# Kernel optimization log

Hardware: AMD Instinct MI355X
Metric: run time of the kernel (lower is better)

Reference implementation:

```python
import jax, jax.numpy as jnp
import numpy as np

B, H, P, S = 512, 4, 196, 256  # batch, heads, pixels, states
D = S // H  # head_state = 64


def conv1x1(x, w, b):
    # x: (B, C_in, P), w: (C_out, C_in), b: (C_out,) -> (B, C_out, P)
    return jnp.einsum('oc,bcp->bop', w, x) + b[None, :, None]


def setup_inputs() -> dict:
    key = jax.random.key(0)
    ks = jax.random.split(key, 9)
    sc = 1.0 / np.sqrt(S)
    return {
        'x': jax.random.normal(ks[0], (B, S, P), dtype=jnp.float32),
        'wq': jax.random.normal(ks[1], (S, S), dtype=jnp.float32) * sc,
        'bq': jax.random.normal(ks[2], (S,), dtype=jnp.float32) * 0.01,
        'wk': jax.random.normal(ks[3], (S, S), dtype=jnp.float32) * sc,
        'bk': jax.random.normal(ks[4], (S,), dtype=jnp.float32) * 0.01,
        'wv': jax.random.normal(ks[5], (S, S), dtype=jnp.float32) * sc,
        'bv': jax.random.normal(ks[6], (S,), dtype=jnp.float32) * 0.01,
        'wo': jax.random.normal(ks[7], (S, S), dtype=jnp.float32) * sc,
        'bo': jax.random.normal(ks[8], (S,), dtype=jnp.float32) * 0.01,
    }


def reference(x, wq, bq, wk, bk, wv, bv, wo, bo):
    def split_heads(t):  # (B, S, P) -> (B, H, P, D)
        return t.reshape(B, H, D, P).swapaxes(-1, -2)

    q = split_heads(conv1x1(x, wq, bq))
    k = split_heads(conv1x1(x, wk, bk))
    v = split_heads(conv1x1(x, wv, bv))

    att = jnp.einsum('bhqd,bhkd->bhqk', q, k) / np.sqrt(D).astype(jnp.float32)
    att = jax.nn.softmax(att, axis=-1)
    av = jnp.einsum('bhqk,bhkd->bhqd', att, v)  # (B, H, P, D)

    # Faithful to original: raw view (B,H,P,D) -> (B,P,S) with NO head transpose
    merged = av.reshape(B, P, S).swapaxes(-1, -2)  # (B, S, P)
    return conv1x1(merged, wo, bo)
```

## Files before the change

kernel.cpp:

```cpp
#include <hip/hip_runtime.h>
#include <stdint.h>


#define PPIX 196
#define SS   256
#define PPAD 224
#define NTT  14

typedef __attribute__((ext_vector_type(8))) short short8;
typedef __attribute__((ext_vector_type(4))) float f32x4;

#define SZ_REGA 29696
#define OFF_QS  (SZ_REGA)
#define SZ_QKS  (224*72*2)
#define OFF_KS  (OFF_QS + SZ_QKS)
#define OFF_VS  (OFF_KS + SZ_QKS)
#define SZ_VS   (64*232*2)
#define OFF_AVS (OFF_VS + SZ_VS)
#define SZ_AVS  32768
#define SMEM_TOTAL (OFF_AVS + SZ_AVS)

static __device__ __forceinline__ uint16_t f2b(float f) {
  uint32_t u = __float_as_uint(f);
  return (uint16_t)((u + 0x7fffu + ((u >> 16) & 1u)) >> 16);
}
static __device__ __forceinline__ f32x4 fz4() {
  f32x4 v; v[0] = 0.f; v[1] = 0.f; v[2] = 0.f; v[3] = 0.f; return v;
}

extern "C" __global__ void __launch_bounds__(256, 1)
mha_fused(const float* __restrict__ x,
          const float* __restrict__ wq, const float* __restrict__ bq,
          const float* __restrict__ wk, const float* __restrict__ bk,
          const float* __restrict__ wv, const float* __restrict__ bv,
          const float* __restrict__ wo, const float* __restrict__ bo,
          float* __restrict__ out) {
  extern __shared__ char smem[];
  uint16_t* const regA = (uint16_t*)(smem);
  uint16_t* const qs   = (uint16_t*)(smem + OFF_QS);
  uint16_t* const ks   = (uint16_t*)(smem + OFF_KS);
  uint16_t* const vsm  = (uint16_t*)(smem + OFF_VS);
  uint16_t* const avs  = (uint16_t*)(smem + OFF_AVS);

  const int bid = blockIdx.x;
  const int L = (bid & 7) * 256 + (bid >> 3);
  const int b = L >> 2, h = L & 3;
  const int tid = threadIdx.x;
  const int w = tid >> 6;
  const int lane = tid & 63;
  const int g = lane >> 4;
  const int l15 = lane & 15;

  const float* xb = x + (size_t)b * (SS * PPIX);

  f32x4 acc1[3][NTT];
#pragma unroll
  for (int mi = 0; mi < 3; ++mi)
#pragma unroll
    for (int nt = 0; nt < NTT; ++nt) acc1[mi][nt] = fz4();

  for (int cc = 0; cc < 4; ++cc) {
    __syncthreads();
    if (tid < PPAD) {
      const int p = tid;
      const int swz = (p & 7) << 3;
      uint32_t* dst = (uint32_t*)(regA + p * 64);
      if (p < PPIX) {
        const float* src = xb + (size_t)(cc * 64) * PPIX + p;
#pragma unroll
        for (int i = 0; i < 32; ++i) {
          float a0 = src[(2 * i) * PPIX];
          float a1 = src[(2 * i + 1) * PPIX];
          uint32_t pk = (uint32_t)f2b(a0) | ((uint32_t)f2b(a1) << 16);
          dst[((2 * i) ^ swz) >> 1] = pk;
        }
      } else {
#pragma unroll
        for (int i = 0; i < 32; ++i) dst[((2 * i) ^ swz) >> 1] = 0u;
      }
    }
    __syncthreads();
#pragma unroll
    for (int kt = 0; kt < 2; ++kt) {
      short8 afr[3];
#pragma unroll
      for (int mi = 0; mi < 3; ++mi) {
        const int mt = 3 * w + mi;
        const int chA = 16 * mt + l15;
        const int mat = chA >> 6;
        const int dA = chA & 63;
        const float* W = (mat == 0) ? wq : ((mat == 1) ? wk : wv);
        const float* srcA = W + (size_t)(h * 64 + dA) * SS + cc * 64 + kt * 32 + g * 8;
        f32x4 w0 = *(const f32x4*)srcA;
        f32x4 w1 = *(const f32x4*)(srcA + 4);
        short8 af;
#pragma unroll
        for (int j = 0; j < 4; ++j) { af[j] = (short)f2b(w0[j]); af[4 + j] = (short)f2b(w1[j]); }
        afr[mi] = af;
      }
#pragma unroll
      for (int nt = 0; nt < NTT; ++nt) {
        const int p = 16 * nt + l15;
        const int coff = (kt * 32 + g * 8) ^ ((p & 7) << 3);
        short8 bfr = *(const short8*)(regA + p * 64 + coff);
#pragma unroll
        for (int mi = 0; mi < 3; ++mi)
          acc1[mi][nt] = __builtin_amdgcn_mfma_f32_16x16x32_bf16(afr[mi], bfr, acc1[mi][nt], 0, 0, 0);
      }
    }
  }
#pragma unroll
  for (int mi = 0; mi < 3; ++mi) {
    const int mt = 3 * w + mi;
    const int mat = (16 * mt) >> 6;
    const float* bias = (mat == 0) ? bq : ((mat == 1) ? bk : bv);
#pragma unroll
    for (int r = 0; r < 4; ++r) {
      const int ch = 16 * mt + 4 * g + r;
      const int d = ch - 64 * mat;
      const float bias_v = bias[h * 64 + d];
#pragma unroll
      for (int nt = 0; nt < NTT; ++nt) {
        const int p = 16 * nt + l15;
        const uint16_t val = f2b(acc1[mi][nt][r] + bias_v);
        if (mat == 2)      vsm[d * 232 + p] = val;
        else if (mat == 0) qs[p * 72 + d]   = val;
        else               ks[p * 72 + d]   = val;
      }
    }
  }
  __syncthreads();

  uint16_t* const psw = regA + w * (16 * 232);
  for (int rt = w; rt < NTT; rt += 4) {
    if (16 * rt >= PPIX) continue;
    f32x4 accA[NTT];
#pragma unroll
    for (int nt = 0; nt < NTT; ++nt) accA[nt] = fz4();
#pragma unroll
    for (int kt = 0; kt < 2; ++kt) {
      short8 a = *(const short8*)(qs + (16 * rt + l15) * 72 + kt * 32 + g * 8);
#pragma unroll
      for (int nt = 0; nt < NTT; ++nt) {
        short8 bfr = *(const short8*)(ks + (16 * nt + l15) * 72 + kt * 32 + g * 8);
        accA[nt] = __builtin_amdgcn_mfma_f32_16x16x32_bf16(a, bfr, accA[nt], 0, 0, 0);
      }
    }
    float mx[4] = {-1e30f, -1e30f, -1e30f, -1e30f};
#pragma unroll
    for (int nt = 0; nt < NTT; ++nt) {
      const int col = 16 * nt + l15;
#pragma unroll
      for (int r = 0; r < 4; ++r) {
        float v = accA[nt][r] * 0.125f;
        if (col >= PPIX) v = -1e30f;
        accA[nt][r] = v;
        mx[r] = fmaxf(mx[r], v);
      }
    }
#pragma unroll
    for (int off = 1; off <= 8; off <<= 1)
#pragma unroll
      for (int r = 0; r < 4; ++r)
        mx[r] = fmaxf(mx[r], __shfl_xor(mx[r], off, 64));
    float sm[4] = {0.f, 0.f, 0.f, 0.f};
#pragma unroll
    for (int nt = 0; nt < NTT; ++nt)
#pragma unroll
      for (int r = 0; r < 4; ++r) {
        float e = exp2f((accA[nt][r] - mx[r]) * 1.44269504088896f);
        accA[nt][r] = e;
        sm[r] += e;
      }
#pragma unroll
    for (int off = 1; off <= 8; off <<= 1)
#pragma unroll
      for (int r = 0; r < 4; ++r)
        sm[r] += __shfl_xor(sm[r], off, 64);
#pragma unroll
    for (int nt = 0; nt < NTT; ++nt)
#pragma unroll
      for (int r = 0; r < 4; ++r)
        psw[(4 * g + r) * 232 + 16 * nt + l15] = f2b(accA[nt][r]);
    f32x4 accV[4];
#pragma unroll
    for (int n = 0; n < 4; ++n) accV[n] = fz4();
#pragma unroll
    for (int kt = 0; kt < 7; ++kt) {
      short8 a = *(const short8*)(psw + l15 * 232 + kt * 32 + g * 8);
#pragma unroll
      for (int n = 0; n < 4; ++n) {
        short8 bfr = *(const short8*)(vsm + (16 * n + l15) * 232 + kt * 32 + g * 8);
        accV[n] = __builtin_amdgcn_mfma_f32_16x16x32_bf16(a, bfr, accV[n], 0, 0, 0);
      }
    }
#pragma unroll
    for (int r = 0; r < 4; ++r) {
      const int p = 16 * rt + 4 * g + r;
      if (p < PPIX) {
        const float inv = 1.0f / sm[r];
        const int swzp = ((p >> 2) & 7) << 3;
#pragma unroll
        for (int n = 0; n < 4; ++n) {
          const int d = 16 * n + l15;
          avs[p * 64 + (d ^ swzp)] = f2b(accV[n][r] * inv);
        }
      }
    }
  }
  __syncthreads();

  f32x4 accO[4][4];
#pragma unroll
  for (int mi = 0; mi < 4; ++mi)
#pragma unroll
    for (int ni = 0; ni < 4; ++ni) accO[mi][ni] = fz4();
#pragma unroll
  for (int kt = 0; kt < 8; ++kt) {
    short8 a[4];
#pragma unroll
    for (int mi = 0; mi < 4; ++mi) {
      const int o = 64 * w + 16 * mi + l15;
      const float* srcA = wo + (size_t)o * SS + kt * 32 + g * 8;
      f32x4 w0 = *(const f32x4*)srcA;
      f32x4 w1 = *(const f32x4*)(srcA + 4);
      short8 af;
#pragma unroll
      for (int j = 0; j < 4; ++j) { af[j] = (short)f2b(w0[j]); af[4 + j] = (short)f2b(w1[j]); }
      a[mi] = af;
    }
#pragma unroll
    for (int ni = 0; ni < 4; ++ni) {
      const int pp = 16 * ni + l15;
      const int s0 = kt * 32 + g * 8;
      const int idx = 256 * pp + ((s0 >> 6) << 6) + ((s0 & 63) ^ ((pp & 7) << 3));
      short8 bfr = *(const short8*)(avs + idx);
#pragma unroll
      for (int mi = 0; mi < 4; ++mi)
        accO[mi][ni] = __builtin_amdgcn_mfma_f32_16x16x32_bf16(a[mi], bfr, accO[mi][ni], 0, 0, 0);
    }
  }
#pragma unroll
  for (int mi = 0; mi < 4; ++mi) {
#pragma unroll
    for (int r = 0; r < 4; ++r) {
      const int o = 64 * w + 16 * mi + 4 * g + r;
      const float bias_v = bo[o];
      float* orow = out + ((size_t)b * SS + o) * PPIX + 49 * h;
#pragma unroll
      for (int ni = 0; ni < 4; ++ni) {
        const int pp = 16 * ni + l15;
        if (pp < 49) orow[pp] = accO[mi][ni][r] + bias_v;
      }
    }
  }
}

extern "C" void kernel_launch(void* const* d_in, const int* in_sizes, int n_in,
                              void* d_out, int out_size, void* d_ws, size_t ws_size,
                              hipStream_t stream) {
  (void)in_sizes; (void)n_in; (void)d_ws; (void)ws_size; (void)out_size;
  const float* x  = (const float*)d_in[0];
  const float* wq = (const float*)d_in[1];
  const float* bq = (const float*)d_in[2];
  const float* wk = (const float*)d_in[3];
  const float* bk = (const float*)d_in[4];
  const float* wv = (const float*)d_in[5];
  const float* bv = (const float*)d_in[6];
  const float* wo = (const float*)d_in[7];
  const float* bo = (const float*)d_in[8];
  float* out = (float*)d_out;
  (void)hipFuncSetAttribute(reinterpret_cast<const void*>(mha_fused),
                            hipFuncAttributeMaxDynamicSharedMemorySize, SMEM_TOTAL);
  mha_fused<<<dim3(2048), dim3(256), SMEM_TOTAL, stream>>>(x, wq, bq, wk, bk, wv, bv, wo, bo, out);
}
```

Baseline: 616.3 us.

## Double threads per block, prepack bf16 weights, and shrink LDS for two blocks per CU

Blocks go from 256 to 512 threads, and the QKV projection work is split across pixel halves as well as channel tiles. The out-projection is split across 8 warps. LDS is shrunk (smaller padded Q/K/V buffers, half-split P staging with a swizzle) so two blocks fit per CU, with launch bounds raised to (512,2). A prepack kernel converts all weights to bf16 in workspace once per call, so the main kernel loads bf16 directly instead of converting fp32 per block. The softmax scale is folded into the exp2 constant. The trade-off is more register pressure per thread and one extra kernel launch.

```diff
diff --git a/kernel.cpp b/kernel.cpp
--- a/kernel.cpp
+++ b/kernel.cpp
@@ -4,20 +4,19 @@
 
 #define PPIX 196
 #define SS   256
-#define PPAD 224
-#define NTT  14
 
 typedef __attribute__((ext_vector_type(8))) short short8;
 typedef __attribute__((ext_vector_type(4))) float f32x4;
 
-#define SZ_REGA 29696
-#define OFF_QS  (SZ_REGA)
-#define SZ_QKS  (224*72*2)
-#define OFF_KS  (OFF_QS + SZ_QKS)
-#define OFF_VS  (OFF_KS + SZ_QKS)
-#define SZ_VS   (64*232*2)
+#define PSWP    144
+#define SZ_UNI  36864
+#define OFF_QS  (SZ_UNI)
+#define SZ_QK   (208*72*2)
+#define OFF_KS  (OFF_QS + SZ_QK)
+#define OFF_VS  (OFF_KS + SZ_QK)
+#define SZ_VS   (64*236*2)
 #define OFF_AVS (OFF_VS + SZ_VS)
-#define SZ_AVS  32768
+#define SZ_AVS  (12544*2)
 #define SMEM_TOTAL (OFF_AVS + SZ_AVS)
 
 static __device__ __forceinline__ uint16_t f2b(float f) {
@@ -28,19 +27,21 @@
   f32x4 v; v[0] = 0.f; v[1] = 0.f; v[2] = 0.f; v[3] = 0.f; return v;
 }
 
-extern "C" __global__ void __launch_bounds__(256, 1)
-mha_fused(const float* __restrict__ x,
-          const float* __restrict__ wq, const float* __restrict__ bq,
-          const float* __restrict__ wk, const float* __restrict__ bk,
-          const float* __restrict__ wv, const float* __restrict__ bv,
-          const float* __restrict__ wo, const float* __restrict__ bo,
-          float* __restrict__ out) {
+template<bool PRE>
+__global__ __launch_bounds__(512, 2)
+void mha_fused(const float* __restrict__ x,
+               const float* __restrict__ wq, const float* __restrict__ bq,
+               const float* __restrict__ wk, const float* __restrict__ bk,
+               const float* __restrict__ wv, const float* __restrict__ bv,
+               const float* __restrict__ wo, const float* __restrict__ bo,
+               const uint16_t* __restrict__ wpk,
+               float* __restrict__ out) {
   extern __shared__ char smem[];
-  uint16_t* const regA = (uint16_t*)(smem);
-  uint16_t* const qs   = (uint16_t*)(smem + OFF_QS);
-  uint16_t* const ks   = (uint16_t*)(smem + OFF_KS);
-  uint16_t* const vsm  = (uint16_t*)(smem + OFF_VS);
-  uint16_t* const avs  = (uint16_t*)(smem + OFF_AVS);
+  uint16_t* const uni = (uint16_t*)(smem);
+  uint16_t* const qs  = (uint16_t*)(smem + OFF_QS);
+  uint16_t* const ks  = (uint16_t*)(smem + OFF_KS);
+  uint16_t* const vsm = (uint16_t*)(smem + OFF_VS);
+  uint16_t* const avs = (uint16_t*)(smem + OFF_AVS);
 
   const int bid = blockIdx.x;
   const int L = (bid & 7) * 256 + (bid >> 3);
@@ -50,110 +51,123 @@
   const int lane = tid & 63;
   const int g = lane >> 4;
   const int l15 = lane & 15;
+  const int wm = w & 3;
+  const int wn = w >> 2;
 
   const float* xb = x + (size_t)b * (SS * PPIX);
 
-  f32x4 acc1[3][NTT];
+  f32x4 acc1[3][7];
 #pragma unroll
   for (int mi = 0; mi < 3; ++mi)
 #pragma unroll
-    for (int nt = 0; nt < NTT; ++nt) acc1[mi][nt] = fz4();
+    for (int nt = 0; nt < 7; ++nt) acc1[mi][nt] = fz4();
+
+  const int prow = tid >> 1;
+  const int phalf = tid & 1;
 
   for (int cc = 0; cc < 4; ++cc) {
     __syncthreads();
-    if (tid < PPAD) {
-      const int p = tid;
-      const int swz = (p & 7) << 3;
-      uint32_t* dst = (uint32_t*)(regA + p * 64);
-      if (p < PPIX) {
-        const float* src = xb + (size_t)(cc * 64) * PPIX + p;
-#pragma unroll
-        for (int i = 0; i < 32; ++i) {
-          float a0 = src[(2 * i) * PPIX];
-          float a1 = src[(2 * i + 1) * PPIX];
-          uint32_t pk = (uint32_t)f2b(a0) | ((uint32_t)f2b(a1) << 16);
-          dst[((2 * i) ^ swz) >> 1] = pk;
+    short8 afr[2][3];
+#pragma unroll
+    for (int kt = 0; kt < 2; ++kt)
+#pragma unroll
+      for (int mi = 0; mi < 3; ++mi) {
+        const int chA = 48 * wm + 16 * mi + l15;
+        const int mat = chA >> 6, dA = chA & 63;
+        const int col = cc * 64 + kt * 32 + g * 8;
+        if (PRE) {
+          afr[kt][mi] = *(const short8*)(wpk + ((size_t)(mat * 256 + h * 64 + dA)) * SS + col);
+        } else {
+          const float* W = (mat == 0) ? wq : ((mat == 1) ? wk : wv);
+          const float* s = W + (size_t)(h * 64 + dA) * SS + col;
+          f32x4 w0 = *(const f32x4*)s, w1 = *(const f32x4*)(s + 4);
+          short8 af;
+#pragma unroll
+          for (int j = 0; j < 4; ++j) { af[j] = (short)f2b(w0[j]); af[4 + j] = (short)f2b(w1[j]); }
+          afr[kt][mi] = af;
+        }
+      }
+    if (prow < 224) {
+      const int swz = (prow & 7) << 3;
+      uint16_t* dstrow = uni + prow * 64;
+      if (prow < PPIX) {
+        const float* src = xb + (size_t)(cc * 64 + phalf * 32) * PPIX + prow;
+#pragma unroll
+        for (int cb = 0; cb < 4; ++cb) {
+          short8 pk;
+#pragma unroll
+          for (int t = 0; t < 8; ++t) pk[t] = (short)f2b(src[(cb * 8 + t) * PPIX]);
+          *(short8*)(dstrow + ((phalf * 32 + cb * 8) ^ swz)) = pk;
         }
       } else {
-#pragma unroll
-        for (int i = 0; i < 32; ++i) dst[((2 * i) ^ swz) >> 1] = 0u;
+        short8 z;
+#pragma unroll
+        for (int t = 0; t < 8; ++t) z[t] = 0;
+#pragma unroll
+        for (int cb = 0; cb < 4; ++cb)
+          *(short8*)(dstrow + ((phalf * 32 + cb * 8) ^ swz)) = z;
       }
     }
     __syncthreads();
 #pragma unroll
-    for (int kt = 0; kt < 2; ++kt) {
-      short8 afr[3];
-#pragma unroll
-      for (int mi = 0; mi < 3; ++mi) {
-        const int mt = 3 * w + mi;
-        const int chA = 16 * mt + l15;
-        const int mat = chA >> 6;
-        const int dA = chA & 63;
-        const float* W = (mat == 0) ? wq : ((mat == 1) ? wk : wv);
-        const float* srcA = W + (size_t)(h * 64 + dA) * SS + cc * 64 + kt * 32 + g * 8;
-        f32x4 w0 = *(const f32x4*)srcA;
-        f32x4 w1 = *(const f32x4*)(srcA + 4);
-        short8 af;
-#pragma unroll
-        for (int j = 0; j < 4; ++j) { af[j] = (short)f2b(w0[j]); af[4 + j] = (short)f2b(w1[j]); }
-        afr[mi] = af;
-      }
-#pragma unroll
-      for (int nt = 0; nt < NTT; ++nt) {
-        const int p = 16 * nt + l15;
+    for (int kt = 0; kt < 2; ++kt)
+#pragma unroll
+      for (int ntl = 0; ntl < 7; ++ntl) {
+        const int p = 16 * (7 * wn + ntl) + l15;
         const int coff = (kt * 32 + g * 8) ^ ((p & 7) << 3);
-        short8 bfr = *(const short8*)(regA + p * 64 + coff);
+        short8 bfr = *(const short8*)(uni + p * 64 + coff);
 #pragma unroll
         for (int mi = 0; mi < 3; ++mi)
-          acc1[mi][nt] = __builtin_amdgcn_mfma_f32_16x16x32_bf16(afr[mi], bfr, acc1[mi][nt], 0, 0, 0);
-      }
-    }
+          acc1[mi][ntl] = __builtin_amdgcn_mfma_f32_16x16x32_bf16(afr[kt][mi], bfr, acc1[mi][ntl], 0, 0, 0);
+      }
   }
 #pragma unroll
   for (int mi = 0; mi < 3; ++mi) {
-    const int mt = 3 * w + mi;
-    const int mat = (16 * mt) >> 6;
+    const int ch0 = 48 * wm + 16 * mi;
+    const int mat = ch0 >> 6;
     const float* bias = (mat == 0) ? bq : ((mat == 1) ? bk : bv);
 #pragma unroll
     for (int r = 0; r < 4; ++r) {
-      const int ch = 16 * mt + 4 * g + r;
-      const int d = ch - 64 * mat;
+      const int ch = ch0 + 4 * g + r;
+      const int d = ch & 63;
       const float bias_v = bias[h * 64 + d];
 #pragma unroll
-      for (int nt = 0; nt < NTT; ++nt) {
-        const int p = 16 * nt + l15;
-        const uint16_t val = f2b(acc1[mi][nt][r] + bias_v);
-        if (mat == 2)      vsm[d * 232 + p] = val;
-        else if (mat == 0) qs[p * 72 + d]   = val;
-        else               ks[p * 72 + d]   = val;
+      for (int ntl = 0; ntl < 7; ++ntl) {
+        const int p = 16 * (7 * wn + ntl) + l15;
+        const uint16_t val = f2b(acc1[mi][ntl][r] + bias_v);
+        if (mat == 2)      vsm[d * 236 + p] = val;
+        else if (mat == 0) { if (p < 208) qs[p * 72 + d] = val; }
+        else               { if (p < 208) ks[p * 72 + d] = val; }
       }
     }
   }
   __syncthreads();
 
-  uint16_t* const psw = regA + w * (16 * 232);
-  for (int rt = w; rt < NTT; rt += 4) {
-    if (16 * rt >= PPIX) continue;
-    f32x4 accA[NTT];
-#pragma unroll
-    for (int nt = 0; nt < NTT; ++nt) accA[nt] = fz4();
+  uint16_t* const psw = uni + w * (16 * PSWP);
+#pragma unroll 1
+  for (int round = 0; round < 2; ++round) {
+    const int rt = 8 * round + w;
+    if (rt > 12) continue;
+    f32x4 accA[14];
+#pragma unroll
+    for (int nt = 0; nt < 14; ++nt) accA[nt] = fz4();
 #pragma unroll
     for (int kt = 0; kt < 2; ++kt) {
       short8 a = *(const short8*)(qs + (16 * rt + l15) * 72 + kt * 32 + g * 8);
 #pragma unroll
-      for (int nt = 0; nt < NTT; ++nt) {
+      for (int nt = 0; nt < 14; ++nt) {
         short8 bfr = *(const short8*)(ks + (16 * nt + l15) * 72 + kt * 32 + g * 8);
         accA[nt] = __builtin_amdgcn_mfma_f32_16x16x32_bf16(a, bfr, accA[nt], 0, 0, 0);
       }
     }
-    float mx[4] = {-1e30f, -1e30f, -1e30f, -1e30f};
-#pragma unroll
-    for (int nt = 0; nt < NTT; ++nt) {
+    float mx[4] = {-3e38f, -3e38f, -3e38f, -3e38f};
+#pragma unroll
+    for (int nt = 0; nt < 14; ++nt) {
       const int col = 16 * nt + l15;
 #pragma unroll
       for (int r = 0; r < 4; ++r) {
-        float v = accA[nt][r] * 0.125f;
-        if (col >= PPIX) v = -1e30f;
+        float v = accA[nt][r];
+        if (col >= PPIX) v = -3e38f;
         accA[nt][r] = v;
         mx[r] = fmaxf(mx[r], v);
       }
@@ -164,11 +178,12 @@
       for (int r = 0; r < 4; ++r)
         mx[r] = fmaxf(mx[r], __shfl_xor(mx[r], off, 64));
     float sm[4] = {0.f, 0.f, 0.f, 0.f};
-#pragma unroll
-    for (int nt = 0; nt < NTT; ++nt)
+    const float cs = 0.125f * 1.44269504088896f;
+#pragma unroll
+    for (int nt = 0; nt < 14; ++nt)
 #pragma unroll
       for (int r = 0; r < 4; ++r) {
-        float e = exp2f((accA[nt][r] - mx[r]) * 1.44269504088896f);
+        float e = exp2f((accA[nt][r] - mx[r]) * cs);
         accA[nt][r] = e;
         sm[r] += e;
       }
@@ -177,20 +192,39 @@
 #pragma unroll
       for (int r = 0; r < 4; ++r)
         sm[r] += __shfl_xor(sm[r], off, 64);
-#pragma unroll
-    for (int nt = 0; nt < NTT; ++nt)
-#pragma unroll
-      for (int r = 0; r < 4; ++r)
-        psw[(4 * g + r) * 232 + 16 * nt + l15] = f2b(accA[nt][r]);
+
     f32x4 accV[4];
 #pragma unroll
     for (int n = 0; n < 4; ++n) accV[n] = fz4();
 #pragma unroll
-    for (int kt = 0; kt < 7; ++kt) {
-      short8 a = *(const short8*)(psw + l15 * 232 + kt * 32 + g * 8);
+    for (int nt = 0; nt < 8; ++nt)
+#pragma unroll
+      for (int r = 0; r < 4; ++r) {
+        const int row = 4 * g + r;
+        psw[row * PSWP + ((16 * nt + l15) ^ ((row & 7) << 3))] = f2b(accA[nt][r]);
+      }
+#pragma unroll
+    for (int kt = 0; kt < 4; ++kt) {
+      short8 a = *(const short8*)(psw + l15 * PSWP + ((kt * 32 + g * 8) ^ ((l15 & 7) << 3)));
 #pragma unroll
       for (int n = 0; n < 4; ++n) {
-        short8 bfr = *(const short8*)(vsm + (16 * n + l15) * 232 + kt * 32 + g * 8);
+        short8 bfr = *(const short8*)(vsm + (16 * n + l15) * 236 + kt * 32 + g * 8);
+        accV[n] = __builtin_amdgcn_mfma_f32_16x16x32_bf16(a, bfr, accV[n], 0, 0, 0);
+      }
+    }
+#pragma unroll
+    for (int nt = 8; nt < 14; ++nt)
+#pragma unroll
+      for (int r = 0; r < 4; ++r) {
+        const int row = 4 * g + r;
+        psw[row * PSWP + ((16 * (nt - 8) + l15) ^ ((row & 7) << 3))] = f2b(accA[nt][r]);
+      }
+#pragma unroll
+    for (int kt = 0; kt < 3; ++kt) {
+      short8 a = *(const short8*)(psw + l15 * PSWP + ((kt * 32 + g * 8) ^ ((l15 & 7) << 3)));
+#pragma unroll
+      for (int n = 0; n < 4; ++n) {
+        short8 bfr = *(const short8*)(vsm + (16 * n + l15) * 236 + 128 + kt * 32 + g * 8);
         accV[n] = __builtin_amdgcn_mfma_f32_16x16x32_bf16(a, bfr, accV[n], 0, 0, 0);
       }
     }
@@ -210,41 +244,46 @@
   }
   __syncthreads();
 
-  f32x4 accO[4][4];
-#pragma unroll
-  for (int mi = 0; mi < 4; ++mi)
+  f32x4 accO[2][4];
+#pragma unroll
+  for (int mi = 0; mi < 2; ++mi)
 #pragma unroll
     for (int ni = 0; ni < 4; ++ni) accO[mi][ni] = fz4();
 #pragma unroll
   for (int kt = 0; kt < 8; ++kt) {
-    short8 a[4];
-#pragma unroll
-    for (int mi = 0; mi < 4; ++mi) {
-      const int o = 64 * w + 16 * mi + l15;
-      const float* srcA = wo + (size_t)o * SS + kt * 32 + g * 8;
-      f32x4 w0 = *(const f32x4*)srcA;
-      f32x4 w1 = *(const f32x4*)(srcA + 4);
-      short8 af;
-#pragma unroll
-      for (int j = 0; j < 4; ++j) { af[j] = (short)f2b(w0[j]); af[4 + j] = (short)f2b(w1[j]); }
-      a[mi] = af;
+    short8 a[2];
+#pragma unroll
+    for (int mi = 0; mi < 2; ++mi) {
+      const int o = 32 * w + 16 * mi + l15;
+      if (PRE) {
+        a[mi] = *(const short8*)(wpk + 3 * 65536 + (size_t)o * SS + kt * 32 + g * 8);
+      } else {
+        const float* srcA = wo + (size_t)o * SS + kt * 32 + g * 8;
+        f32x4 w0 = *(const f32x4*)srcA;
+        f32x4 w1 = *(const f32x4*)(srcA + 4);
+        short8 af;
+#pragma unroll
+        for (int j = 0; j < 4; ++j) { af[j] = (short)f2b(w0[j]); af[4 + j] = (short)f2b(w1[j]); }
+        a[mi] = af;
+      }
     }
 #pragma unroll
     for (int ni = 0; ni < 4; ++ni) {
       const int pp = 16 * ni + l15;
+      const int pmin = pp < 49 ? pp : 48;
       const int s0 = kt * 32 + g * 8;
-      const int idx = 256 * pp + ((s0 >> 6) << 6) + ((s0 & 63) ^ ((pp & 7) << 3));
+      const int idx = 256 * pmin + ((s0 >> 6) << 6) + ((s0 & 63) ^ ((pmin & 7) << 3));
       short8 bfr = *(const short8*)(avs + idx);
 #pragma unroll
-      for (int mi = 0; mi < 4; ++mi)
+      for (int mi = 0; mi < 2; ++mi)
         accO[mi][ni] = __builtin_amdgcn_mfma_f32_16x16x32_bf16(a[mi], bfr, accO[mi][ni], 0, 0, 0);
     }
   }
 #pragma unroll
-  for (int mi = 0; mi < 4; ++mi) {
+  for (int mi = 0; mi < 2; ++mi) {
 #pragma unroll
     for (int r = 0; r < 4; ++r) {
-      const int o = 64 * w + 16 * mi + 4 * g + r;
+      const int o = 32 * w + 16 * mi + 4 * g + r;
       const float bias_v = bo[o];
       float* orow = out + ((size_t)b * SS + o) * PPIX + 49 * h;
 #pragma unroll
@@ -256,10 +295,26 @@
   }
 }
 
+__global__ __launch_bounds__(256)
+void prepack_w(const float* __restrict__ wq, const float* __restrict__ wk,
+               const float* __restrict__ wv, const float* __restrict__ wo,
+               uint16_t* __restrict__ ws) {
+  const int t = blockIdx.x * 256 + threadIdx.x;
+  const int mat = t >> 13;
+  const int off = (t & 8191) << 3;
+  const float* src = (mat == 0) ? wq : ((mat == 1) ? wk : ((mat == 2) ? wv : wo));
+  f32x4 a = *(const f32x4*)(src + off);
+  f32x4 b = *(const f32x4*)(src + off + 4);
+  short8 o;
+#pragma unroll
+  for (int j = 0; j < 4; ++j) { o[j] = (short)f2b(a[j]); o[4 + j] = (short)f2b(b[j]); }
+  *(short8*)(ws + ((size_t)mat << 16) + off) = o;
+}
+
 extern "C" void kernel_launch(void* const* d_in, const int* in_sizes, int n_in,
                               void* d_out, int out_size, void* d_ws, size_t ws_size,
                               hipStream_t stream) {
-  (void)in_sizes; (void)n_in; (void)d_ws; (void)ws_size; (void)out_size;
+  (void)in_sizes; (void)n_in; (void)out_size;
   const float* x  = (const float*)d_in[0];
   const float* wq = (const float*)d_in[1];
   const float* bq = (const float*)d_in[2];
@@ -270,7 +325,19 @@
   const float* wo = (const float*)d_in[7];
   const float* bo = (const float*)d_in[8];
   float* out = (float*)d_out;
-  (void)hipFuncSetAttribute(reinterpret_cast<const void*>(mha_fused),
-                            hipFuncAttributeMaxDynamicSharedMemorySize, SMEM_TOTAL);
-  mha_fused<<<dim3(2048), dim3(256), SMEM_TOTAL, stream>>>(x, wq, bq, wk, bk, wv, bv, wo, bo, out);
-}
+  uint16_t* ws16 = (uint16_t*)d_ws;
+
+  const bool pre = (d_ws != nullptr) && (ws_size >= (size_t)4 * 65536 * sizeof(uint16_t));
+  if (pre) {
+    (void)hipFuncSetAttribute(reinterpret_cast<const void*>(&mha_fused<true>),
+                              hipFuncAttributeMaxDynamicSharedMemorySize, SMEM_TOTAL);
+    prepack_w<<<dim3(128), dim3(256), 0, stream>>>(wq, wk, wv, wo, ws16);
+    mha_fused<true><<<dim3(2048), dim3(512), SMEM_TOTAL, stream>>>(
+        x, wq, bq, wk, bk, wv, bv, wo, bo, ws16, out);
+  } else {
+    (void)hipFuncSetAttribute(reinterpret_cast<const void*>(&mha_fused<false>),
+                              hipFuncAttributeMaxDynamicSharedMemorySize, SMEM_TOTAL);
+    mha_fused<false><<<dim3(2048), dim3(512), SMEM_TOTAL, stream>>>(
+        x, wq, bq, wk, bk, wv, bv, wo, bo, ws16, out);
+  }
+}
```

Result: faster. 545.0 us (-11.6%).
